# Performance work log

Measured on AMD Instinct MI355X. Metric: run time of the kernel, lower is better.

Reference implementation:

```python
import jax, jax.numpy as jnp
import numpy as np

B, S, SE, D, H, FF, E, K = 2, 2048, 2048, 1024, 16, 4096, 8, 2
HD = D // H


def setup_inputs() -> dict:
    key = jax.random.key(0)
    ks = jax.random.split(key, 32)
    w = lambda k, shape: jax.random.normal(k, shape, jnp.float32) * 0.02
    inp = {
        'x': jax.random.normal(ks[0], (B, S, D), jnp.float32),
        'encoder_output': jax.random.normal(ks[1], (B, SE, D), jnp.float32),
        # causal self-attention projections
        'sa_wq': w(ks[2], (D, D)), 'sa_bq': jnp.zeros((D,), jnp.float32),
        'sa_wk': w(ks[3], (D, D)), 'sa_bk': jnp.zeros((D,), jnp.float32),
        'sa_wv': w(ks[4], (D, D)), 'sa_bv': jnp.zeros((D,), jnp.float32),
        'sa_wo': w(ks[5], (D, D)), 'sa_bo': jnp.zeros((D,), jnp.float32),
        # cross-attention projections
        'ca_wq': w(ks[6], (D, D)), 'ca_bq': jnp.zeros((D,), jnp.float32),
        'ca_wk': w(ks[7], (D, D)), 'ca_bk': jnp.zeros((D,), jnp.float32),
        'ca_wv': w(ks[8], (D, D)), 'ca_bv': jnp.zeros((D,), jnp.float32),
        'ca_wo': w(ks[9], (D, D)), 'ca_bo': jnp.zeros((D,), jnp.float32),
        # layernorms
        'ln1_g': jnp.ones((D,), jnp.float32), 'ln1_b': jnp.zeros((D,), jnp.float32),
        'ln2_g': jnp.ones((D,), jnp.float32), 'ln2_b': jnp.zeros((D,), jnp.float32),
        'ln3_g': jnp.ones((D,), jnp.float32), 'ln3_b': jnp.zeros((D,), jnp.float32),
        # router + experts
        'router_w': w(ks[10], (D, E)), 'router_b': jnp.zeros((E,), jnp.float32),
        'e_w1': w(ks[11], (E, D, FF)), 'e_b1': jnp.zeros((E, FF), jnp.float32),
        'e_w2': w(ks[12], (E, FF, D)), 'e_b2': jnp.zeros((E, D), jnp.float32),
    }
    return inp


def _layernorm(x, g, b):
    m = x.mean(-1, keepdims=True)
    v = ((x - m) ** 2).mean(-1, keepdims=True)
    return (x - m) / jnp.sqrt(v + 1e-5) * g + b


def _attn(q_in, k_in, v_in, wq, bq, wk, bk, wv, bv, wo, bo, causal):
    Bq, Sq, Dm = q_in.shape
    Sk = k_in.shape[1]
    Q = (q_in @ wq + bq).reshape(Bq, Sq, H, HD)
    Kp = (k_in @ wk + bk).reshape(Bq, Sk, H, HD)
    V = (v_in @ wv + bv).reshape(Bq, Sk, H, HD)
    scores = jnp.einsum('bqhd,bkhd->bhqk', Q, Kp) / jnp.sqrt(jnp.float32(HD))
    if causal:
        mask = jnp.tril(jnp.ones((Sq, Sk), bool))
        scores = jnp.where(mask, scores, -jnp.inf)
    a = jax.nn.softmax(scores, axis=-1)
    o = jnp.einsum('bhqk,bkhd->bqhd', a, V).reshape(Bq, Sq, Dm)
    return o @ wo + bo


def _moe(x, rw, rb, w1, b1, w2, b2):
    T = x.shape[0] * x.shape[1]
    xf = x.reshape(T, D)
    router_weights = jax.nn.softmax(xf @ rw + rb, axis=-1)          # [T,E]
    topw, topi = jax.lax.top_k(router_weights, K)                   # [T,K]
    topw = jax.nn.softmax(topw, axis=-1)                            # renormalize top-k
    # combine[t,e] = sum_k topw[t,k] * (topi[t,k]==e)
    combine = jnp.zeros((T, E), xf.dtype).at[jnp.arange(T)[:, None], topi].add(topw)
    # dense compute over all experts (same math as masked dispatch)
    h = jax.nn.gelu(jnp.einsum('td,edf->etf', xf, w1) + b1[:, None, :], approximate=False)
    eo = jnp.einsum('etf,efd->etd', h, w2) + b2[:, None, :]          # [E,T,D]
    out = jnp.einsum('etd,te->td', eo, combine)
    return out.reshape(x.shape)


def reference(x, encoder_output,
              sa_wq, sa_bq, sa_wk, sa_bk, sa_wv, sa_bv, sa_wo, sa_bo,
              ca_wq, ca_bq, ca_wk, ca_bk, ca_wv, ca_bv, ca_wo, ca_bo,
              ln1_g, ln1_b, ln2_g, ln2_b, ln3_g, ln3_b,
              router_w, router_b, e_w1, e_b1, e_w2, e_b2):
    x = _layernorm(x + _attn(x, x, x, sa_wq, sa_bq, sa_wk, sa_bk, sa_wv, sa_bv, sa_wo, sa_bo, True), ln1_g, ln1_b)
    x = _layernorm(x + _attn(x, encoder_output, encoder_output, ca_wq, ca_bq, ca_wk, ca_bk, ca_wv, ca_bv, ca_wo, ca_bo, False), ln2_g, ln2_b)
    x = _layernorm(x + _moe(x, router_w, router_b, e_w1, e_b1, e_w2, e_b2), ln3_g, ln3_b)
    return x
```

## Files before the change

kernel.cpp:

```cpp
#include <hip/hip_runtime.h>

typedef unsigned short u16;
typedef unsigned int   u32;
typedef __bf16    bf16x8 __attribute__((ext_vector_type(8)));
typedef _Float16  f16x8  __attribute__((ext_vector_type(8)));
typedef _Float16  f16x4  __attribute__((ext_vector_type(4)));
typedef __fp16    fp16x2 __attribute__((ext_vector_type(2)));
typedef float     f32x4  __attribute__((ext_vector_type(4)));
typedef u16       u16x4  __attribute__((ext_vector_type(4)));

#define DEV static __device__ __forceinline__

#if __has_builtin(__builtin_amdgcn_mfma_f32_16x16x16f16)
#define HAVE_MFMA16 1
#else
#define HAVE_MFMA16 0
#endif

constexpr int DIMc  = 1024;
constexpr int NHEAD = 16;
constexpr int HDM   = 64;
constexpr int SLENc = 2048;
constexpr int NBAT  = 2;
constexpr int NTOK  = NBAT * SLENc;
constexpr int FFD   = 4096;
constexpr int NEXP  = 8;
constexpr int NSLOT = 2 * NTOK;
constexpr long TD   = (long)NTOK * DIMc;
constexpr float RSC = 2048.0f;
constexpr float RSCI = 1.0f / 2048.0f;

DEV u16 f2bf(float f) {
  u32 u = __float_as_uint(f);
  u += 0x7fffu + ((u >> 16) & 1u);
  return (u16)(u >> 16);
}
DEV float bf2f(u16 h) { return __uint_as_float(((u32)h) << 16); }
DEV float h2f(u16 u) { union { _Float16 h; u16 u_; } x; x.u_ = u; return (float)x.h; }

DEV void split2v(float v, u16& h, u16& r) {
  _Float16 hh = (_Float16)v;
  float rf = (v - (float)hh) * RSC;
  union { _Float16 h_; u16 u_; } a, b;
  a.h_ = hh; b.h_ = (_Float16)rf;
  h = a.u_; r = b.u_;
}

DEV u32 pkrtz(float a, float b) {
  union { fp16x2 v; u32 u; } x;
  x.v = __builtin_amdgcn_cvt_pkrtz(a, b);
  return x.u;
}

DEV f16x4 mk4(u32 lo, u32 hi) {
  union { u32 u[2]; f16x4 v; } x;
  x.u[0] = lo; x.u[1] = hi;
  return x.v;
}

DEV void async16(const void* g, void* l) {
  __builtin_amdgcn_global_load_lds((const u32*)g, (u32*)l, 16, 0, 0);
}

DEV f32x4 mfma_bf(bf16x8 a, bf16x8 b, f32x4 c) {
  return __builtin_amdgcn_mfma_f32_16x16x32_bf16(a, b, c, 0, 0, 0);
}
DEV f32x4 mfma_h(f16x8 a, f16x8 b, f32x4 c) {
  return __builtin_amdgcn_mfma_f32_16x16x32_f16(a, b, c, 0, 0, 0);
}
#if HAVE_MFMA16
DEV f32x4 mfma16h(f16x4 a, f16x4 b, f32x4 c) {
  return __builtin_amdgcn_mfma_f32_16x16x16f16(a, b, c, 0, 0, 0);
}
#endif

DEV f16x8 ldfragh(const u16 (*T)[64], int row, int blk) {
  return *(const f16x8*)((const u16*)T + row * 64 + ((blk ^ (row & 7)) * 8));
}
DEV f16x4 ldVfrag4(const u16 (*T)[64], int row, int kn, int kc) {
  const int blk = kn * 2 + (kc >> 1);
  const u16* p = (const u16*)T + row * 64 + ((blk ^ (row & 7)) * 8) + (kc & 1) * 4;
  return *(const f16x4*)p;
}

DEV float gelu_fast(float v) {
  float arg = v * fmaf(0.044715f * v, v, 1.0f) * 0.7978845608028654f;
  return v / (1.0f + __expf(-2.0f * arg));
}

__global__ __launch_bounds__(256) void split2_kernel(
    const float* __restrict__ x, u16* __restrict__ o0, u16* __restrict__ o1, long n) {
  long i = ((long)blockIdx.x * 256 + threadIdx.x) * 4;
  if (i >= n) return;
  f32x4 v = *(const f32x4*)(x + i);
  u16x4 h, r;
#pragma unroll
  for (int j = 0; j < 4; ++j) { u16 a, b; split2v(v[j], a, b); h[j] = a; r[j] = b; }
  *(u16x4*)(o0 + i) = h;
  *(u16x4*)(o1 + i) = r;
}

__global__ __launch_bounds__(256) void wsplit2_kernel(
    const float* __restrict__ W, u16* __restrict__ t0, u16* __restrict__ t1, int R, int C) {
  __shared__ alignas(16) float tile[32][33];
  const long base = (long)blockIdx.z * R * C;
  const int c0 = blockIdx.x * 32, r0 = blockIdx.y * 32;
  const int tx = threadIdx.x & 31, ty = threadIdx.x >> 5;
#pragma unroll
  for (int i = 0; i < 32; i += 8)
    tile[ty + i][tx] = W[base + (long)(r0 + ty + i) * C + (c0 + tx)];
  __syncthreads();
#pragma unroll
  for (int i = 0; i < 32; i += 8) {
    float v = tile[tx][ty + i];
    long oidx = base + (long)(c0 + ty + i) * R + (r0 + tx);
    u16 a, b; split2v(v, a, b);
    t0[oidx] = a; t1[oidx] = b;
  }
}

__global__ __launch_bounds__(256) void wsplit1_kernel(
    const float* __restrict__ W, u16* __restrict__ t0, int R, int C) {
  __shared__ alignas(16) float tile[32][33];
  const long base = (long)blockIdx.z * R * C;
  const int c0 = blockIdx.x * 32, r0 = blockIdx.y * 32;
  const int tx = threadIdx.x & 31, ty = threadIdx.x >> 5;
#pragma unroll
  for (int i = 0; i < 32; i += 8)
    tile[ty + i][tx] = W[base + (long)(r0 + ty + i) * C + (c0 + tx)];
  __syncthreads();
#pragma unroll
  for (int i = 0; i < 32; i += 8) {
    long oidx = base + (long)(c0 + ty + i) * R + (r0 + tx);
    t0[oidx] = f2bf(tile[tx][ty + i]);
  }
}

__global__ __launch_bounds__(256) void biascat_kernel(
    const float* __restrict__ q, const float* __restrict__ k, const float* __restrict__ v,
    const float* __restrict__ ck, const float* __restrict__ cv,
    float* __restrict__ qkvb, float* __restrict__ kvb) {
  int i = blockIdx.x * 256 + threadIdx.x;
  if (i < 1024) qkvb[i] = q[i];
  else if (i < 2048) qkvb[i] = k[i - 1024];
  else if (i < 3072) qkvb[i] = v[i - 2048];
  else if (i < 4096) kvb[i - 3072] = ck[i - 3072];
  else if (i < 5120) kvb[i - 3072] = cv[i - 4096];
}

__global__ __launch_bounds__(256) void vtrans2_kernel(
    const u16* __restrict__ vh, const u16* __restrict__ vr, int ld,
    u16* __restrict__ t0, u16* __restrict__ t1) {
  __shared__ alignas(16) float tile[32][33];
  const int bh = blockIdx.z, b = bh >> 4, h = bh & 15;
  const int s0 = blockIdx.x * 32, d0 = blockIdx.y * 32;
  const int tx = threadIdx.x & 31, ty = threadIdx.x >> 5;
#pragma unroll
  for (int i = 0; i < 32; i += 8) {
    long idx = (long)(b * SLENc + s0 + ty + i) * ld + h * HDM + d0 + tx;
    tile[ty + i][tx] = h2f(vh[idx]) + h2f(vr[idx]) * RSCI;
  }
  __syncthreads();
#pragma unroll
  for (int i = 0; i < 32; i += 8) {
    float v = tile[tx][ty + i];
    long o = ((long)bh * HDM + d0 + ty + i) * SLENc + s0 + tx;
    u16 a, b_; split2v(v, a, b_);
    t0[o] = a; t1[o] = b_;
  }
}

template<int MT, int BK, bool SPLIT, bool GATHER, int EPI>
__global__ __launch_bounds__(256) void gemm_kernel(
    const u16* __restrict__ A0, const u16* __restrict__ A1,
    const u16* __restrict__ B0, const u16* __restrict__ B1,
    const float* __restrict__ bias, void* __restrict__ Cout, u16* __restrict__ C1,
    int M, int N, int Kd,
    const int* __restrict__ tlist, const int* __restrict__ cnts, const int* __restrict__ offs) {
  constexpr int NP   = SPLIT ? 2 : 1;
  constexpr int NBUF = (BK == 32) ? 2 : 1;
  constexpr int RPC  = 512 / BK;
  constexpr int ACH  = (MT / RPC) / 4;
  constexpr int BCH  = (128 / RPC) / 4;
  constexpr int MREP = MT / 32;
  constexpr int WRS  = MT / 2;
  __shared__ alignas(16) u16 As[NBUF][NP][MT * BK];
  __shared__ alignas(16) u16 Bs[NBUF][NP][128 * BK];

  const int e   = blockIdx.z;
  const int cnt = cnts ? cnts[e] : M;
  const int off = offs ? offs[e] : 0;
  const int m0  = blockIdx.y * MT;
  if (m0 >= cnt) return;
  const int n0  = blockIdx.x * 128;

  const int tid = threadIdx.x;
  const int lane = tid & 63, wid = tid >> 6;
  const int fr = lane & 15, kc = lane >> 4;
  const int wr = wid >> 1, wc = wid & 1;

  const long boff = (long)e * N * Kd;

  int srow, kseg8;
  if constexpr (BK == 32) { srow = lane >> 2; kseg8 = lane & 3; }
  else                    { srow = lane >> 3; kseg8 = (lane & 7) ^ (srow & 7); }

  long aoff[ACH], boff_[BCH];
#pragma unroll
  for (int c = 0; c < ACH; ++c) {
    const int row = (wid * ACH + c) * RPC + srow;
    long ar;
    if (GATHER) {
      int idx = m0 + row; if (idx >= cnt) idx = cnt - 1;
      ar = tlist[off + idx];
    } else {
      ar = (long)(off + m0 + row);
    }
    aoff[c] = ar * Kd + kseg8 * 8;
  }
#pragma unroll
  for (int c = 0; c < BCH; ++c) {
    const int row = (wid * BCH + c) * RPC + srow;
    boff_[c] = boff + (long)(n0 + row) * Kd + kseg8 * 8;
  }

  f32x4 acc[MREP][4], acc1[MREP][4];
#pragma unroll
  for (int m = 0; m < MREP; ++m)
#pragma unroll
    for (int n = 0; n < 4; ++n) { acc[m][n] = f32x4{0.f,0.f,0.f,0.f}; acc1[m][n] = f32x4{0.f,0.f,0.f,0.f}; }

  auto stage = [&](int kt, int bufi) {
    const int k0 = kt * BK;
#pragma unroll
    for (int c = 0; c < ACH; ++c) {
      const int chunk = wid * ACH + c;
      async16(A0 + aoff[c] + k0, &As[bufi][0][chunk * 512]);
      if constexpr (SPLIT) async16(A1 + aoff[c] + k0, &As[bufi][1][chunk * 512]);
    }
#pragma unroll
    for (int c = 0; c < BCH; ++c) {
      const int chunk = wid * BCH + c;
      async16(B0 + boff_[c] + k0, &Bs[bufi][0][chunk * 512]);
      if constexpr (SPLIT) async16(B1 + boff_[c] + k0, &Bs[bufi][1][chunk * 512]);
    }
  };

  auto compute = [&](int bufi) {
    if constexpr (BK == 32) {
      if constexpr (SPLIT) {
        f16x8 a0[MREP], a1[MREP];
#pragma unroll
        for (int m = 0; m < MREP; ++m) {
          const int idx = (wr * WRS + m * 16 + fr) * 32 + kc * 8;
          a0[m] = *(const f16x8*)&As[bufi][0][idx];
          a1[m] = *(const f16x8*)&As[bufi][1][idx];
        }
#pragma unroll
        for (int n = 0; n < 4; ++n) {
          const int idx = (wc * 64 + n * 16 + fr) * 32 + kc * 8;
          f16x8 b0 = *(const f16x8*)&Bs[bufi][0][idx];
          f16x8 b1 = *(const f16x8*)&Bs[bufi][1][idx];
#pragma unroll
          for (int m = 0; m < MREP; ++m) {
            acc[m][n]  = mfma_h(a0[m], b0, acc[m][n]);
            acc1[m][n] = mfma_h(a0[m], b1, acc1[m][n]);
            acc1[m][n] = mfma_h(a1[m], b0, acc1[m][n]);
          }
        }
      } else {
        bf16x8 a0[MREP];
#pragma unroll
        for (int m = 0; m < MREP; ++m)
          a0[m] = *(const bf16x8*)&As[bufi][0][(wr * WRS + m * 16 + fr) * 32 + kc * 8];
#pragma unroll
        for (int n = 0; n < 4; ++n) {
          bf16x8 b0 = *(const bf16x8*)&Bs[bufi][0][(wc * 64 + n * 16 + fr) * 32 + kc * 8];
#pragma unroll
          for (int m = 0; m < MREP; ++m)
            acc[m][n] = mfma_bf(a0[m], b0, acc[m][n]);
        }
      }
    } else {
#pragma unroll
      for (int ksub = 0; ksub < 2; ++ksub) {
        bf16x8 a0[MREP];
#pragma unroll
        for (int m = 0; m < MREP; ++m) {
          const int row = wr * WRS + m * 16 + fr;
          a0[m] = *(const bf16x8*)&As[0][0][row * 64 + (((ksub << 2) | kc) ^ (fr & 7)) * 8];
        }
#pragma unroll
        for (int n = 0; n < 4; ++n) {
          const int row = wc * 64 + n * 16 + fr;
          bf16x8 b0 = *(const bf16x8*)&Bs[0][0][row * 64 + (((ksub << 2) | kc) ^ (fr & 7)) * 8];
#pragma unroll
          for (int m = 0; m < MREP; ++m)
            acc[m][n] = mfma_bf(a0[m], b0, acc[m][n]);
        }
      }
    }
  };

  const int NK = Kd / BK;
  if constexpr (BK == 32) {
    stage(0, 0);
    int cur = 0;
    for (int kt = 0; kt < NK; ++kt) {
      __syncthreads();
      if (kt + 1 < NK) stage(kt + 1, cur ^ 1);
      compute(cur);
      cur ^= 1;
    }
  } else {
    for (int kt = 0; kt < NK; ++kt) {
      __syncthreads();
      stage(kt, 0);
      __syncthreads();
      compute(0);
    }
  }

  const float* bvec = bias + (long)e * N;
#pragma unroll
  for (int m = 0; m < MREP; ++m) {
#pragma unroll
    for (int j = 0; j < 4; ++j) {
      const int r = m0 + wr * WRS + m * 16 + kc * 4 + j;
      if (r >= cnt) continue;
      const long orow = (long)(off + r) * N;
#pragma unroll
      for (int n = 0; n < 4; ++n) {
        const int col = n0 + wc * 64 + n * 16 + fr;
        float v = acc[m][n][j];
        if constexpr (SPLIT) v += acc1[m][n][j] * RSCI;
        v += bvec[col];
        if constexpr (EPI == 0) {
          ((float*)Cout)[orow + col] = v;
        } else if constexpr (EPI == 1) {
          ((u16*)Cout)[orow + col] = f2bf(gelu_fast(v));
        } else if constexpr (EPI == 2) {
          ((u16*)Cout)[orow + col] = f2bf(v);
        } else {
          u16 a_, b_; split2v(v, a_, b_);
          ((u16*)Cout)[orow + col] = a_;
          C1[orow + col] = b_;
        }
      }
    }
  }
}

#if !HAVE_MFMA16
DEV f16x8 gather_fragh(u32 a0, u32 a1, u32 b0, u32 b1, int lane) {
  const int kc = lane >> 4;
  const int base = (lane & 15) + ((kc & 1) << 5);
  union { u32 u[4]; f16x8 v; } r;
  u32 s00 = (u32)__shfl((int)a0, base, 64);
  u32 s01 = (u32)__shfl((int)a1, base, 64);
  u32 s10 = (u32)__shfl((int)b0, base, 64);
  u32 s11 = (u32)__shfl((int)b1, base, 64);
  u32 t00 = (u32)__shfl((int)a0, base + 16, 64);
  u32 t01 = (u32)__shfl((int)a1, base + 16, 64);
  u32 t10 = (u32)__shfl((int)b0, base + 16, 64);
  u32 t11 = (u32)__shfl((int)b1, base + 16, 64);
  const bool hi = (kc >> 1) != 0;
  r.u[0] = hi ? s10 : s00;
  r.u[1] = hi ? s11 : s01;
  r.u[2] = hi ? t10 : t00;
  r.u[3] = hi ? t11 : t01;
  return r.v;
}
#endif

template<bool CAUSAL>
__global__ __launch_bounds__(256, 2) void attn2_kernel(
    const u16* __restrict__ Qh, const u16* __restrict__ Qr, int qld,
    const u16* __restrict__ Kh, const u16* __restrict__ Kr, int kld,
    const u16* __restrict__ Vh, const u16* __restrict__ Vr,
    u16* __restrict__ OH, u16* __restrict__ OR) {
  __shared__ alignas(16) u16 KQs[2][2][64][64];
  __shared__ alignas(16) u16 Vts[2][2][64][64];

  const int qt = CAUSAL ? ((int)gridDim.x - 1 - (int)blockIdx.x) : (int)blockIdx.x;
  const int h = blockIdx.y, b = blockIdx.z;
  const int tid = threadIdx.x, lane = tid & 63, w = tid >> 6;
  const int fr = lane & 15, kc = lane >> 4;
  const int q0 = qt * 64;
  const long qbase = (long)(b * SLENc) * qld + h * HDM;
  const long kbase = (long)(b * SLENc) * kld + h * HDM;
  const long obase = (long)(b * SLENc) * DIMc + h * HDM;
  const long vtbase = (long)(b * NHEAD + h) * HDM * SLENc;
  const int r = lane >> 3, blk = (lane & 7) ^ r;

  auto stageKV = [&](int kt, int bufi) {
#pragma unroll
    for (int p = 0; p < 2; ++p) {
      const u16* gp = (p == 0 ? Kh : Kr);
#pragma unroll
      for (int cc = 0; cc < 2; ++cc) {
        int c = w + 4 * cc;
        async16(gp + kbase + (long)(kt * 64 + 8 * c + r) * kld + blk * 8, &KQs[bufi][p][8 * c][0]);
      }
    }
    const long vrow = vtbase + kt * 64;
#pragma unroll
    for (int p = 0; p < 2; ++p) {
      const u16* gp = (p == 0 ? Vh : Vr);
#pragma unroll
      for (int cc = 0; cc < 2; ++cc) {
        int c = w + 4 * cc;
        async16(gp + vrow + (long)(8 * c + r) * SLENc + blk * 8, &Vts[bufi][p][8 * c][0]);
      }
    }
  };

#pragma unroll
  for (int p = 0; p < 2; ++p) {
    const u16* gp = (p == 0 ? Qh : Qr);
#pragma unroll
    for (int cc = 0; cc < 2; ++cc) {
      int c = w + 4 * cc;
      async16(gp + qbase + (long)(q0 + 8 * c + r) * qld + blk * 8, &KQs[0][p][8 * c][0]);
    }
  }
  __syncthreads();
  f16x8 qf0[2], qf1[2];
#pragma unroll
  for (int s = 0; s < 2; ++s) {
    qf0[s] = ldfragh(KQs[0][0], w * 16 + fr, s * 4 + kc);
    qf1[s] = ldfragh(KQs[0][1], w * 16 + fr, s * 4 + kc);
  }
  stageKV(0, 1);

  f32x4 accO0[4], accO1[4];
#pragma unroll
  for (int dn = 0; dn < 4; ++dn) { accO0[dn] = f32x4{0.f,0.f,0.f,0.f}; accO1[dn] = f32x4{0.f,0.f,0.f,0.f}; }
  float m_ = -3e38f, l_ = 0.f;

  const int nkt = CAUSAL ? (qt + 1) : (SLENc / 64);
  int cur = 1;
  for (int kt = 0; kt < nkt; ++kt) {
    __syncthreads();
    if (kt + 1 < nkt) stageKV(kt + 1, cur ^ 1);

    f32x4 sc0[4], sc1[4];
#pragma unroll
    for (int kn = 0; kn < 4; ++kn) { sc0[kn] = f32x4{0.f,0.f,0.f,0.f}; sc1[kn] = f32x4{0.f,0.f,0.f,0.f}; }
    __builtin_amdgcn_s_setprio(1);
#pragma unroll
    for (int kn = 0; kn < 4; ++kn)
#pragma unroll
      for (int s = 0; s < 2; ++s) {
        f16x8 ah = ldfragh(KQs[cur][0], kn * 16 + fr, s * 4 + kc);
        f16x8 ar = ldfragh(KQs[cur][1], kn * 16 + fr, s * 4 + kc);
        sc0[kn] = mfma_h(ah, qf0[s], sc0[kn]);
        sc1[kn] = mfma_h(ah, qf1[s], sc1[kn]);
        sc1[kn] = mfma_h(ar, qf0[s], sc1[kn]);
      }
    __builtin_amdgcn_s_setprio(0);

    constexpr float SCL = 0.125f, SCL2 = 0.125f * RSCI;
    float p_[4][4];
    float mx = -3e38f;
#pragma unroll
    for (int kn = 0; kn < 4; ++kn)
#pragma unroll
      for (int j = 0; j < 4; ++j) {
        float sv = fmaf(sc0[kn][j], SCL, sc1[kn][j] * SCL2);
        if (CAUSAL && kt == qt) {
          if (kn * 16 + kc * 4 + j > w * 16 + fr) sv = -3e38f;
        }
        p_[kn][j] = sv;
        mx = fmaxf(mx, sv);
      }
    mx = fmaxf(mx, __shfl_xor(mx, 16, 64));
    mx = fmaxf(mx, __shfl_xor(mx, 32, 64));
    if (!__all(mx <= m_ + 8.f)) {
      const float mn = fmaxf(m_, mx);
      const float corr = __expf(m_ - mn);
      m_ = mn;
      l_ *= corr;
#pragma unroll
      for (int dn = 0; dn < 4; ++dn) { accO0[dn] *= corr; accO1[dn] *= corr; }
    }
    float rs = 0.f;
#pragma unroll
    for (int kn = 0; kn < 4; ++kn)
#pragma unroll
      for (int j = 0; j < 4; ++j) {
        float p = __expf(p_[kn][j] - m_);
        p_[kn][j] = p;
        rs += p;
      }
    rs += __shfl_xor(rs, 16, 64);
    rs += __shfl_xor(rs, 32, 64);
    l_ += rs;

#if HAVE_MFMA16
#pragma unroll
    for (int kn = 0; kn < 4; ++kn) {
      u32 hp0 = pkrtz(p_[kn][0], p_[kn][1]);
      u32 hp1 = pkrtz(p_[kn][2], p_[kn][3]);
      float h0 = h2f((u16)hp0), h1 = h2f((u16)(hp0 >> 16));
      float h2_ = h2f((u16)hp1), h3 = h2f((u16)(hp1 >> 16));
      u32 rp0 = pkrtz((p_[kn][0] - h0) * RSC, (p_[kn][1] - h1) * RSC);
      u32 rp1 = pkrtz((p_[kn][2] - h2_) * RSC, (p_[kn][3] - h3) * RSC);
      f16x4 ph = mk4(hp0, hp1), pr = mk4(rp0, rp1);
      __builtin_amdgcn_s_setprio(1);
#pragma unroll
      for (int dn = 0; dn < 4; ++dn) {
        f16x4 vh = ldVfrag4(Vts[cur][0], dn * 16 + fr, kn, kc);
        f16x4 vr = ldVfrag4(Vts[cur][1], dn * 16 + fr, kn, kc);
        accO0[dn] = mfma16h(vh, ph, accO0[dn]);
        accO1[dn] = mfma16h(vh, pr, accO1[dn]);
        accO1[dn] = mfma16h(vr, ph, accO1[dn]);
      }
      __builtin_amdgcn_s_setprio(0);
    }
#else
    u32 hpk[4][2], rpk[4][2];
#pragma unroll
    for (int kn = 0; kn < 4; ++kn)
#pragma unroll
      for (int jp = 0; jp < 2; ++jp) {
        float p0 = p_[kn][2 * jp], p1 = p_[kn][2 * jp + 1];
        u32 hp = pkrtz(p0, p1);
        float h0 = h2f((u16)hp), h1 = h2f((u16)(hp >> 16));
        u32 rp = pkrtz((p0 - h0) * RSC, (p1 - h1) * RSC);
        hpk[kn][jp] = hp;
        rpk[kn][jp] = rp;
      }
#pragma unroll
    for (int s = 0; s < 2; ++s) {
      f16x8 ph = gather_fragh(hpk[2 * s][0], hpk[2 * s][1], hpk[2 * s + 1][0], hpk[2 * s + 1][1], lane);
      f16x8 pr = gather_fragh(rpk[2 * s][0], rpk[2 * s][1], rpk[2 * s + 1][0], rpk[2 * s + 1][1], lane);
      __builtin_amdgcn_s_setprio(1);
#pragma unroll
      for (int dn = 0; dn < 4; ++dn) {
        f16x8 vh = ldfragh(Vts[cur][0], dn * 16 + fr, s * 4 + kc);
        f16x8 vr = ldfragh(Vts[cur][1], dn * 16 + fr, s * 4 + kc);
        accO0[dn] = mfma_h(vh, ph, accO0[dn]);
        accO1[dn] = mfma_h(vh, pr, accO1[dn]);
        accO1[dn] = mfma_h(vr, ph, accO1[dn]);
      }
      __builtin_amdgcn_s_setprio(0);
    }
#endif
    cur ^= 1;
  }

  const float inv = 1.0f / l_;
#pragma unroll
  for (int dn = 0; dn < 4; ++dn) {
    u16x4 hv, rv;
#pragma unroll
    for (int j = 0; j < 4; ++j) {
      float o = (accO0[dn][j] + accO1[dn][j] * RSCI) * inv;
      u16 a_, b_; split2v(o, a_, b_);
      hv[j] = a_; rv[j] = b_;
    }
    const long oidx = obase + (long)(q0 + w * 16 + fr) * DIMc + dn * 16 + kc * 4;
    *(u16x4*)&OH[oidx] = hv;
    *(u16x4*)&OR[oidx] = rv;
  }
}

template<int NS>
__global__ __launch_bounds__(256) void resln_kernel(
    const float* __restrict__ resid, const float* __restrict__ proj,
    const float* __restrict__ gam, const float* __restrict__ bet,
    float* __restrict__ yout, u16* __restrict__ s0, u16* __restrict__ s1) {
  __shared__ float red[4];
  const int t = blockIdx.x, tid = threadIdx.x;
  const long base = (long)t * DIMc;
  float v[4];
#pragma unroll
  for (int i = 0; i < 4; ++i) {
    int d = tid + i * 256;
    v[i] = resid[base + d] + proj[base + d];
  }
  float s = v[0] + v[1] + v[2] + v[3];
#pragma unroll
  for (int o = 32; o; o >>= 1) s += __shfl_xor(s, o, 64);
  if ((tid & 63) == 0) red[tid >> 6] = s;
  __syncthreads();
  const float mean = (red[0] + red[1] + red[2] + red[3]) * (1.0f / DIMc);
  __syncthreads();
  float q = 0.f;
#pragma unroll
  for (int i = 0; i < 4; ++i) { float d_ = v[i] - mean; q += d_ * d_; }
#pragma unroll
  for (int o = 32; o; o >>= 1) q += __shfl_xor(q, o, 64);
  if ((tid & 63) == 0) red[tid >> 6] = q;
  __syncthreads();
  const float var = (red[0] + red[1] + red[2] + red[3]) * (1.0f / DIMc);
  const float inv = rsqrtf(var + 1e-5f);
#pragma unroll
  for (int i = 0; i < 4; ++i) {
    int d = tid + i * 256;
    float y = (v[i] - mean) * inv * gam[d] + bet[d];
    yout[base + d] = y;
    if constexpr (NS == 1) s0[base + d] = f2bf(y);
    if constexpr (NS == 2) {
      u16 a, b; split2v(y, a, b);
      s0[base + d] = a; s1[base + d] = b;
    }
  }
}

__global__ __launch_bounds__(256) void resln_router_kernel(
    const float* __restrict__ resid, const float* __restrict__ proj,
    const float* __restrict__ gam, const float* __restrict__ bet,
    const float* __restrict__ rw, const float* __restrict__ rb,
    float* __restrict__ yout, u16* __restrict__ s0,
    int* __restrict__ topi, float* __restrict__ topw, int* __restrict__ cnt) {
  __shared__ float red[4];
  __shared__ float rpart[4][8];
  const int t = blockIdx.x, tid = threadIdx.x;
  const int lane = tid & 63, wv = tid >> 6;
  const long base = (long)t * DIMc;
  float v[4];
#pragma unroll
  for (int i = 0; i < 4; ++i) {
    int d = tid + i * 256;
    v[i] = resid[base + d] + proj[base + d];
  }
  float s = v[0] + v[1] + v[2] + v[3];
#pragma unroll
  for (int o = 32; o; o >>= 1) s += __shfl_xor(s, o, 64);
  if (lane == 0) red[wv] = s;
  __syncthreads();
  const float mean = (red[0] + red[1] + red[2] + red[3]) * (1.0f / DIMc);
  __syncthreads();
  float q = 0.f;
#pragma unroll
  for (int i = 0; i < 4; ++i) { float d_ = v[i] - mean; q += d_ * d_; }
#pragma unroll
  for (int o = 32; o; o >>= 1) q += __shfl_xor(q, o, 64);
  if (lane == 0) red[wv] = q;
  __syncthreads();
  const float var = (red[0] + red[1] + red[2] + red[3]) * (1.0f / DIMc);
  const float inv = rsqrtf(var + 1e-5f);
  float part[8] = {};
#pragma unroll
  for (int i = 0; i < 4; ++i) {
    int d = tid + i * 256;
    float y = (v[i] - mean) * inv * gam[d] + bet[d];
    yout[base + d] = y;
    s0[base + d] = f2bf(y);
    const f32x4* wp = (const f32x4*)&rw[d * 8];
    f32x4 w0 = wp[0], w1 = wp[1];
    part[0] += y * w0[0]; part[1] += y * w0[1]; part[2] += y * w0[2]; part[3] += y * w0[3];
    part[4] += y * w1[0]; part[5] += y * w1[1]; part[6] += y * w1[2]; part[7] += y * w1[3];
  }
#pragma unroll
  for (int o = 32; o; o >>= 1)
#pragma unroll
    for (int e = 0; e < 8; ++e) part[e] += __shfl_xor(part[e], o, 64);
  if (lane == 0)
#pragma unroll
    for (int e = 0; e < 8; ++e) rpart[wv][e] = part[e];
  __syncthreads();
  if (tid == 0) {
    float lg[8];
#pragma unroll
    for (int e = 0; e < 8; ++e)
      lg[e] = rpart[0][e] + rpart[1][e] + rpart[2][e] + rpart[3][e] + rb[e];
    int i1 = 0;
#pragma unroll
    for (int e = 1; e < 8; ++e) if (lg[e] > lg[i1]) i1 = e;
    int i2 = (i1 == 0) ? 1 : 0;
#pragma unroll
    for (int e = 0; e < 8; ++e) if (e != i1 && lg[e] > lg[i2]) i2 = e;
    float mx = lg[i1], ps = 0.f, p[8];
#pragma unroll
    for (int e = 0; e < 8; ++e) { p[e] = __expf(lg[e] - mx); ps += p[e]; }
    float p1 = p[i1] / ps, p2 = p[i2] / ps;
    float e2 = __expf(p2 - p1);
    float w1 = 1.0f / (1.0f + e2);
    topi[t * 2] = i1; topi[t * 2 + 1] = i2;
    topw[t * 2] = w1; topw[t * 2 + 1] = e2 * w1;
    atomicAdd(&cnt[i1], 1); atomicAdd(&cnt[i2], 1);
  }
}

__global__ void scan_kernel(const int* __restrict__ cnt, int* __restrict__ offs, int* __restrict__ pos) {
  if (threadIdx.x == 0) {
    int a = 0;
    for (int e = 0; e < NEXP; ++e) { offs[e] = a; a += cnt[e]; }
  }
  if (threadIdx.x < NEXP) pos[threadIdx.x] = 0;
}

__global__ __launch_bounds__(256) void fill_kernel(
    const int* __restrict__ topi, const int* __restrict__ offs, int* __restrict__ pos,
    int* __restrict__ tlist, int* __restrict__ slotof) {
  int t = blockIdx.x * 256 + threadIdx.x;
  if (t >= NTOK) return;
#pragma unroll
  for (int k = 0; k < 2; ++k) {
    int e = topi[t * 2 + k];
    int pp = atomicAdd(&pos[e], 1);
    int s = offs[e] + pp;
    tlist[s] = t;
    slotof[t * 2 + k] = s;
  }
}

__global__ __launch_bounds__(256) void final_kernel(
    const float* __restrict__ x2, const u16* __restrict__ eo,
    const int* __restrict__ slotof, const float* __restrict__ topw,
    const float* __restrict__ gam, const float* __restrict__ bet, float* __restrict__ out) {
  __shared__ float red[4];
  const int t = blockIdx.x, tid = threadIdx.x;
  const long base = (long)t * DIMc;
  const int s0 = slotof[t * 2], s1 = slotof[t * 2 + 1];
  const float w0 = topw[t * 2], w1 = topw[t * 2 + 1];
  float v[4];
#pragma unroll
  for (int i = 0; i < 4; ++i) {
    int d = tid + i * 256;
    float moe = w0 * bf2f(eo[(long)s0 * DIMc + d]) + w1 * bf2f(eo[(long)s1 * DIMc + d]);
    v[i] = x2[base + d] + moe;
  }
  float s = v[0] + v[1] + v[2] + v[3];
#pragma unroll
  for (int o = 32; o; o >>= 1) s += __shfl_xor(s, o, 64);
  if ((tid & 63) == 0) red[tid >> 6] = s;
  __syncthreads();
  const float mean = (red[0] + red[1] + red[2] + red[3]) * (1.0f / DIMc);
  __syncthreads();
  float q = 0.f;
#pragma unroll
  for (int i = 0; i < 4; ++i) { float d_ = v[i] - mean; q += d_ * d_; }
#pragma unroll
  for (int o = 32; o; o >>= 1) q += __shfl_xor(q, o, 64);
  if ((tid & 63) == 0) red[tid >> 6] = q;
  __syncthreads();
  const float var = (red[0] + red[1] + red[2] + red[3]) * (1.0f / DIMc);
  const float inv = rsqrtf(var + 1e-5f);
#pragma unroll
  for (int i = 0; i < 4; ++i) {
    int d = tid + i * 256;
    out[base + d] = (v[i] - mean) * inv * gam[d] + bet[d];
  }
}

extern "C" void kernel_launch(void* const* d_in, const int* in_sizes, int n_in,
                              void* d_out, int out_size, void* d_ws, size_t ws_size,
                              hipStream_t stream) {
  (void)in_sizes; (void)n_in; (void)out_size; (void)ws_size;
  const float* x     = (const float*)d_in[0];
  const float* enc   = (const float*)d_in[1];
  const float* aw[8] = {(const float*)d_in[2],  (const float*)d_in[4],  (const float*)d_in[6],  (const float*)d_in[8],
                        (const float*)d_in[10], (const float*)d_in[12], (const float*)d_in[14], (const float*)d_in[16]};
  const float* ab[8] = {(const float*)d_in[3],  (const float*)d_in[5],  (const float*)d_in[7],  (const float*)d_in[9],
                        (const float*)d_in[11], (const float*)d_in[13], (const float*)d_in[15], (const float*)d_in[17]};
  const float* ln1_g = (const float*)d_in[18]; const float* ln1_b = (const float*)d_in[19];
  const float* ln2_g = (const float*)d_in[20]; const float* ln2_b = (const float*)d_in[21];
  const float* ln3_g = (const float*)d_in[22]; const float* ln3_b = (const float*)d_in[23];
  const float* rw    = (const float*)d_in[24]; const float* rb    = (const float*)d_in[25];
  const float* e_w1  = (const float*)d_in[26]; const float* e_b1  = (const float*)d_in[27];
  const float* e_w2  = (const float*)d_in[28]; const float* e_b2  = (const float*)d_in[29];

  char* basep = (char*)d_ws;
  size_t offb = 0;
  auto alloc = [&](size_t nbytes) -> void* {
    void* r = basep + offb;
    offb += (nbytes + 255) & ~(size_t)255;
    return r;
  };

  const size_t PLANE_BF = (size_t)TD * 2;
  const size_t PLANE_F  = (size_t)TD * 4;
  const size_t WPLANE   = (size_t)DIMc * DIMc * 2;

  u16 *xs0 = (u16*)alloc(PLANE_BF), *xs1 = (u16*)alloc(PLANE_BF);
  u16 *es0 = (u16*)alloc(PLANE_BF), *es1 = (u16*)alloc(PLANE_BF);
  u16 *os0 = (u16*)alloc(PLANE_BF), *os1 = (u16*)alloc(PLANE_BF);
  u16 *wqkv0 = (u16*)alloc(3 * WPLANE), *wqkv1 = (u16*)alloc(3 * WPLANE);
  u16 *wkv0  = (u16*)alloc(2 * WPLANE), *wkv1  = (u16*)alloc(2 * WPLANE);
  u16 *wq0   = (u16*)alloc(WPLANE),     *wq1   = (u16*)alloc(WPLANE);
  u16 *wo10  = (u16*)alloc(WPLANE),     *wo11  = (u16*)alloc(WPLANE);
  u16 *wo20  = (u16*)alloc(WPLANE),     *wo21  = (u16*)alloc(WPLANE);
  u16* w1t = (u16*)alloc((size_t)NEXP * FFD * DIMc * 2);
  u16* w2t = (u16*)alloc((size_t)NEXP * DIMc * FFD * 2);
  u16 *QKVh = (u16*)alloc(3 * PLANE_BF), *QKVr = (u16*)alloc(3 * PLANE_BF);
  u16 *KVh  = (u16*)alloc(2 * PLANE_BF), *KVr  = (u16*)alloc(2 * PLANE_BF);
  u16 *Qch  = (u16*)alloc(PLANE_BF),     *Qcr  = (u16*)alloc(PLANE_BF);
  u16 *Vth  = (u16*)alloc(PLANE_BF),     *Vtr  = (u16*)alloc(PLANE_BF);
  float* qkvb = (float*)alloc(3072 * 4);
  float* kvb  = (float*)alloc(2048 * 4);
  float* aout = (float*)alloc(PLANE_F);
  float* x1   = (float*)alloc(PLANE_F);
  float* x2   = (float*)alloc(PLANE_F);
  u16*   x2h  = (u16*)alloc(PLANE_BF);
  u16*   hbuf = (u16*)alloc((size_t)(NSLOT + 128) * FFD * 2);
  u16*   eo   = (u16*)alloc((size_t)NSLOT * DIMc * 2);
  int*   topi   = (int*)alloc(NSLOT * 4);
  float* topwp  = (float*)alloc(NSLOT * 4);
  int*   tlist  = (int*)alloc(NSLOT * 4);
  int*   slotof = (int*)alloc(NSLOT * 4);
  int*   cnt    = (int*)alloc(NEXP * 4);
  int*   offs   = (int*)alloc(NEXP * 4);
  int*   pos    = (int*)alloc(NEXP * 4);

  (void)hipMemsetAsync(cnt, 0, NEXP * sizeof(int), stream);

  const int SB = (int)(TD / 4 / 256);
  split2_kernel<<<SB, 256, 0, stream>>>(x, xs0, xs1, TD);
  split2_kernel<<<SB, 256, 0, stream>>>(enc, es0, es1, TD);
  for (int s = 0; s < 3; ++s)
    wsplit2_kernel<<<dim3(32, 32, 1), 256, 0, stream>>>(aw[s], wqkv0 + (size_t)s * DIMc * DIMc, wqkv1 + (size_t)s * DIMc * DIMc, DIMc, DIMc);
  wsplit2_kernel<<<dim3(32, 32, 1), 256, 0, stream>>>(aw[5], wkv0, wkv1, DIMc, DIMc);
  wsplit2_kernel<<<dim3(32, 32, 1), 256, 0, stream>>>(aw[6], wkv0 + (size_t)DIMc * DIMc, wkv1 + (size_t)DIMc * DIMc, DIMc, DIMc);
  wsplit2_kernel<<<dim3(32, 32, 1), 256, 0, stream>>>(aw[4], wq0, wq1, DIMc, DIMc);
  wsplit2_kernel<<<dim3(32, 32, 1), 256, 0, stream>>>(aw[3], wo10, wo11, DIMc, DIMc);
  wsplit2_kernel<<<dim3(32, 32, 1), 256, 0, stream>>>(aw[7], wo20, wo21, DIMc, DIMc);
  wsplit1_kernel<<<dim3(FFD / 32, DIMc / 32, NEXP), 256, 0, stream>>>(e_w1, w1t, DIMc, FFD);
  wsplit1_kernel<<<dim3(DIMc / 32, FFD / 32, NEXP), 256, 0, stream>>>(e_w2, w2t, FFD, DIMc);
  biascat_kernel<<<20, 256, 0, stream>>>(ab[0], ab[1], ab[2], ab[5], ab[6], qkvb, kvb);

  const dim3 gproj(DIMc / 128, NTOK / 64, 1);
  const dim3 gqkv(3 * DIMc / 128, NTOK / 64, 1);
  const dim3 gkv(2 * DIMc / 128, NTOK / 64, 1);
  const dim3 gattn(SLENc / 64, NHEAD, NBAT);
  const dim3 gvt(SLENc / 32, HDM / 32, NBAT * NHEAD);

  gemm_kernel<64, 32, true, false, 3><<<gqkv, 256, 0, stream>>>(xs0, xs1, wqkv0, wqkv1, qkvb, QKVh, QKVr, NTOK, 3 * DIMc, DIMc, nullptr, nullptr, nullptr);
  vtrans2_kernel<<<gvt, 256, 0, stream>>>(QKVh + 2048, QKVr + 2048, 3 * DIMc, Vth, Vtr);
  attn2_kernel<true><<<gattn, 256, 0, stream>>>(QKVh, QKVr, 3 * DIMc, QKVh + 1024, QKVr + 1024, 3 * DIMc, Vth, Vtr, os0, os1);
  gemm_kernel<64, 32, true, false, 0><<<gproj, 256, 0, stream>>>(os0, os1, wo10, wo11, ab[3], aout, nullptr, NTOK, DIMc, DIMc, nullptr, nullptr, nullptr);
  resln_kernel<2><<<NTOK, 256, 0, stream>>>(x, aout, ln1_g, ln1_b, x1, xs0, xs1);
  gemm_kernel<64, 32, true, false, 3><<<gproj, 256, 0, stream>>>(xs0, xs1, wq0, wq1, ab[4], Qch, Qcr, NTOK, DIMc, DIMc, nullptr, nullptr, nullptr);
  gemm_kernel<64, 32, true, false, 3><<<gkv, 256, 0, stream>>>(es0, es1, wkv0, wkv1, kvb, KVh, KVr, NTOK, 2 * DIMc, DIMc, nullptr, nullptr, nullptr);
  vtrans2_kernel<<<gvt, 256, 0, stream>>>(KVh + 1024, KVr + 1024, 2 * DIMc, Vth, Vtr);
  attn2_kernel<false><<<gattn, 256, 0, stream>>>(Qch, Qcr, DIMc, KVh, KVr, 2 * DIMc, Vth, Vtr, os0, os1);
  gemm_kernel<64, 32, true, false, 0><<<gproj, 256, 0, stream>>>(os0, os1, wo20, wo21, ab[7], aout, nullptr, NTOK, DIMc, DIMc, nullptr, nullptr, nullptr);
  resln_router_kernel<<<NTOK, 256, 0, stream>>>(x1, aout, ln2_g, ln2_b, rw, rb, x2, x2h, topi, topwp, cnt);
  scan_kernel<<<1, 64, 0, stream>>>(cnt, offs, pos);
  fill_kernel<<<NTOK / 256, 256, 0, stream>>>(topi, offs, pos, tlist, slotof);
  gemm_kernel<128, 64, false, true, 1><<<dim3(FFD / 128, NTOK / 128, NEXP), 256, 0, stream>>>(
      x2h, nullptr, w1t, nullptr, e_b1, hbuf, nullptr, NTOK, FFD, DIMc, tlist, cnt, offs);
  gemm_kernel<128, 64, false, false, 2><<<dim3(DIMc / 128, NTOK / 128, NEXP), 256, 0, stream>>>(
      hbuf, nullptr, w2t, nullptr, e_b2, eo, nullptr, NTOK, DIMc, FFD, nullptr, cnt, offs);
  final_kernel<<<NTOK, 256, 0, stream>>>(x2, eo, slotof, topwp, ln3_g, ln3_b, (float*)d_out);
}
```

Baseline: 1.187 ms.

## Use 128-query attention tiles with 8 warps sharing each staged K/V tile

```diff
diff --git a/kernel.cpp b/kernel.cpp
--- a/kernel.cpp
+++ b/kernel.cpp
@@ -374,7 +374,7 @@
 #endif
 
 template<bool CAUSAL>
-__global__ __launch_bounds__(256, 2) void attn2_kernel(
+__global__ __launch_bounds__(512, 4) void attn2_kernel(
     const u16* __restrict__ Qh, const u16* __restrict__ Qr, int qld,
     const u16* __restrict__ Kh, const u16* __restrict__ Kr, int kld,
     const u16* __restrict__ Vh, const u16* __restrict__ Vr,
@@ -385,8 +385,11 @@
   const int qt = CAUSAL ? ((int)gridDim.x - 1 - (int)blockIdx.x) : (int)blockIdx.x;
   const int h = blockIdx.y, b = blockIdx.z;
   const int tid = threadIdx.x, lane = tid & 63, w = tid >> 6;
+  const int wq = w >> 2, wl = w & 3;
   const int fr = lane & 15, kc = lane >> 4;
-  const int q0 = qt * 64;
+  const int q0 = qt * 128;
+  const int qrow = wq * 64 + wl * 16 + fr;
+  const int qglob = q0 + qrow;
   const long qbase = (long)(b * SLENc) * qld + h * HDM;
   const long kbase = (long)(b * SLENc) * kld + h * HDM;
   const long obase = (long)(b * SLENc) * DIMc + h * HDM;
@@ -397,39 +400,35 @@
 #pragma unroll
     for (int p = 0; p < 2; ++p) {
       const u16* gp = (p == 0 ? Kh : Kr);
-#pragma unroll
-      for (int cc = 0; cc < 2; ++cc) {
-        int c = w + 4 * cc;
-        async16(gp + kbase + (long)(kt * 64 + 8 * c + r) * kld + blk * 8, &KQs[bufi][p][8 * c][0]);
-      }
+      async16(gp + kbase + (long)(kt * 64 + 8 * w + r) * kld + blk * 8, &KQs[bufi][p][8 * w][0]);
     }
     const long vrow = vtbase + kt * 64;
 #pragma unroll
     for (int p = 0; p < 2; ++p) {
       const u16* gp = (p == 0 ? Vh : Vr);
-#pragma unroll
-      for (int cc = 0; cc < 2; ++cc) {
-        int c = w + 4 * cc;
-        async16(gp + vrow + (long)(8 * c + r) * SLENc + blk * 8, &Vts[bufi][p][8 * c][0]);
-      }
+      async16(gp + vrow + (long)(8 * w + r) * SLENc + blk * 8, &Vts[bufi][p][8 * w][0]);
     }
   };
 
 #pragma unroll
-  for (int p = 0; p < 2; ++p) {
-    const u16* gp = (p == 0 ? Qh : Qr);
-#pragma unroll
-    for (int cc = 0; cc < 2; ++cc) {
-      int c = w + 4 * cc;
-      async16(gp + qbase + (long)(q0 + 8 * c + r) * qld + blk * 8, &KQs[0][p][8 * c][0]);
+  for (int hh = 0; hh < 2; ++hh) {
+#pragma unroll
+    for (int p = 0; p < 2; ++p) {
+      const u16* gp = (p == 0 ? Qh : Qr);
+      u16* dst = hh == 0 ? &KQs[0][p][8 * w][0] : &Vts[0][p][8 * w][0];
+      async16(gp + qbase + (long)(q0 + hh * 64 + 8 * w + r) * qld + blk * 8, dst);
     }
   }
   __syncthreads();
   f16x8 qf0[2], qf1[2];
-#pragma unroll
-  for (int s = 0; s < 2; ++s) {
-    qf0[s] = ldfragh(KQs[0][0], w * 16 + fr, s * 4 + kc);
-    qf1[s] = ldfragh(KQs[0][1], w * 16 + fr, s * 4 + kc);
+  {
+    const u16 (*Q0)[64] = (wq == 0) ? KQs[0][0] : Vts[0][0];
+    const u16 (*Q1)[64] = (wq == 0) ? KQs[0][1] : Vts[0][1];
+#pragma unroll
+    for (int s = 0; s < 2; ++s) {
+      qf0[s] = ldfragh(Q0, wl * 16 + fr, s * 4 + kc);
+      qf1[s] = ldfragh(Q1, wl * 16 + fr, s * 4 + kc);
+    }
   }
   stageKV(0, 1);
 
@@ -438,7 +437,7 @@
   for (int dn = 0; dn < 4; ++dn) { accO0[dn] = f32x4{0.f,0.f,0.f,0.f}; accO1[dn] = f32x4{0.f,0.f,0.f,0.f}; }
   float m_ = -3e38f, l_ = 0.f;
 
-  const int nkt = CAUSAL ? (qt + 1) : (SLENc / 64);
+  const int nkt = CAUSAL ? (2 * qt + 2) : (SLENc / 64);
   int cur = 1;
   for (int kt = 0; kt < nkt; ++kt) {
     __syncthreads();
@@ -468,8 +467,8 @@
 #pragma unroll
       for (int j = 0; j < 4; ++j) {
         float sv = fmaf(sc0[kn][j], SCL, sc1[kn][j] * SCL2);
-        if (CAUSAL && kt == qt) {
-          if (kn * 16 + kc * 4 + j > w * 16 + fr) sv = -3e38f;
+        if (CAUSAL) {
+          if (kt * 64 + kn * 16 + kc * 4 + j > qglob) sv = -3e38f;
         }
         p_[kn][j] = sv;
         mx = fmaxf(mx, sv);
@@ -560,7 +559,7 @@
       u16 a_, b_; split2v(o, a_, b_);
       hv[j] = a_; rv[j] = b_;
     }
-    const long oidx = obase + (long)(q0 + w * 16 + fr) * DIMc + dn * 16 + kc * 4;
+    const long oidx = obase + (long)(q0 + qrow) * DIMc + dn * 16 + kc * 4;
     *(u16x4*)&OH[oidx] = hv;
     *(u16x4*)&OR[oidx] = rv;
   }
@@ -825,18 +824,18 @@
   const dim3 gproj(DIMc / 128, NTOK / 64, 1);
   const dim3 gqkv(3 * DIMc / 128, NTOK / 64, 1);
   const dim3 gkv(2 * DIMc / 128, NTOK / 64, 1);
-  const dim3 gattn(SLENc / 64, NHEAD, NBAT);
+  const dim3 gattn(SLENc / 128, NHEAD, NBAT);
   const dim3 gvt(SLENc / 32, HDM / 32, NBAT * NHEAD);
 
   gemm_kernel<64, 32, true, false, 3><<<gqkv, 256, 0, stream>>>(xs0, xs1, wqkv0, wqkv1, qkvb, QKVh, QKVr, NTOK, 3 * DIMc, DIMc, nullptr, nullptr, nullptr);
   vtrans2_kernel<<<gvt, 256, 0, stream>>>(QKVh + 2048, QKVr + 2048, 3 * DIMc, Vth, Vtr);
-  attn2_kernel<true><<<gattn, 256, 0, stream>>>(QKVh, QKVr, 3 * DIMc, QKVh + 1024, QKVr + 1024, 3 * DIMc, Vth, Vtr, os0, os1);
+  attn2_kernel<true><<<gattn, 512, 0, stream>>>(QKVh, QKVr, 3 * DIMc, QKVh + 1024, QKVr + 1024, 3 * DIMc, Vth, Vtr, os0, os1);
   gemm_kernel<64, 32, true, false, 0><<<gproj, 256, 0, stream>>>(os0, os1, wo10, wo11, ab[3], aout, nullptr, NTOK, DIMc, DIMc, nullptr, nullptr, nullptr);
   resln_kernel<2><<<NTOK, 256, 0, stream>>>(x, aout, ln1_g, ln1_b, x1, xs0, xs1);
   gemm_kernel<64, 32, true, false, 3><<<gproj, 256, 0, stream>>>(xs0, xs1, wq0, wq1, ab[4], Qch, Qcr, NTOK, DIMc, DIMc, nullptr, nullptr, nullptr);
   gemm_kernel<64, 32, true, false, 3><<<gkv, 256, 0, stream>>>(es0, es1, wkv0, wkv1, kvb, KVh, KVr, NTOK, 2 * DIMc, DIMc, nullptr, nullptr, nullptr);
   vtrans2_kernel<<<gvt, 256, 0, stream>>>(KVh + 1024, KVr + 1024, 2 * DIMc, Vth, Vtr);
-  attn2_kernel<false><<<gattn, 256, 0, stream>>>(Qch, Qcr, DIMc, KVh, KVr, 2 * DIMc, Vth, Vtr, os0, os1);
+  attn2_kernel<false><<<gattn, 512, 0, stream>>>(Qch, Qcr, DIMc, KVh, KVr, 2 * DIMc, Vth, Vtr, os0, os1);
   gemm_kernel<64, 32, true, false, 0><<<gproj, 256, 0, stream>>>(os0, os1, wo20, wo21, ab[7], aout, nullptr, NTOK, DIMc, DIMc, nullptr, nullptr, nullptr);
   resln_router_kernel<<<NTOK, 256, 0, stream>>>(x1, aout, ln2_g, ln2_b, rw, rb, x2, x2h, topi, topwp, cnt);
   scan_kernel<<<1, 64, 0, stream>>>(cnt, offs, pos);
```

After: 1.134 ms. -4.5%, faster.
